# Kernel optimization log

Measured on AMD Instinct MI355X. Metric: run time of the kernel, lower is better.

Reference implementation:

```python
import jax, jax.numpy as jnp
import numpy as np

B, S, D = 8, 2048, 256
H, HD = 4, 64  # num_heads, head_size; H*HD == D


def setup_inputs() -> dict:
    key = jax.random.key(0)
    ks = jax.random.split(key, 9)
    scale = 0.02
    return {
        "x": jax.random.normal(ks[0], (B, S, D), dtype=jnp.float32),
        "Wq": jax.random.normal(ks[1], (D, H * HD), dtype=jnp.float32) * scale,
        "bq": jnp.zeros((H * HD,), dtype=jnp.float32),
        "Wk": jax.random.normal(ks[2], (D, H * HD), dtype=jnp.float32) * scale,
        "bk": jnp.zeros((H * HD,), dtype=jnp.float32),
        "Wv": jax.random.normal(ks[3], (D, H * HD), dtype=jnp.float32) * scale,
        "bv": jnp.zeros((H * HD,), dtype=jnp.float32),
        "Wo": jax.random.normal(ks[4], (H * HD, D), dtype=jnp.float32) * scale,
        "bo": jnp.zeros((D,), dtype=jnp.float32),
    }


def _split_heads(t):
    # [B, S, H*HD] -> [B, H, S, HD]
    b, s, _ = t.shape
    return t.reshape(b, s, H, HD).transpose(0, 2, 1, 3)


def reference(x, Wq, bq, Wk, bk, Wv, bv, Wo, bo):
    q = _split_heads(x @ Wq + bq)
    k = _split_heads(x @ Wk + bk)
    v = _split_heads(x @ Wv + bv)
    scores = jnp.einsum("bhqd,bhkd->bhqk", q, k) / jnp.sqrt(jnp.float32(HD))
    weights = jax.nn.softmax(scores, axis=-1)
    attn = jnp.einsum("bhqk,bhkd->bhqd", weights, v)  # [B, H, S, HD]
    concat = attn.transpose(0, 2, 1, 3).reshape(x.shape[0], -1, H * HD)
    return concat @ Wo + bo
```

## Files before the change

kernel.cpp:

```cpp
#include <hip/hip_runtime.h>
#include <hip/hip_bf16.h>

namespace {

constexpr int B_ = 8, S = 2048, D = 256, H = 4, HD = 64;
constexpr int M = B_ * S;

typedef __attribute__((ext_vector_type(8))) short bf16x8;
typedef __attribute__((ext_vector_type(4))) short bf16x4;
typedef __attribute__((ext_vector_type(4))) float f32x4;
typedef __attribute__((ext_vector_type(16))) float f32x16;
typedef __attribute__((ext_vector_type(4))) unsigned uint4v;

__device__ inline short f2bf(float x) {
  __hip_bfloat16 h = __float2bfloat16(x);
  short s;
  __builtin_memcpy(&s, &h, 2);
  return s;
}

__device__ inline f32x4 mfma16(bf16x8 a, bf16x8 b, f32x4 c) {
  return __builtin_amdgcn_mfma_f32_16x16x32_bf16(a, b, c, 0, 0, 0);
}
__device__ inline f32x16 mfma32(bf16x8 a, bf16x8 b, f32x16 c) {
  return __builtin_amdgcn_mfma_f32_32x32x16_bf16(a, b, c, 0, 0, 0);
}

__device__ inline float exp2a(float x) {
  float r;
  asm("v_exp_f32 %0, %1" : "=v"(r) : "v"(x));
  return r;
}

__device__ inline unsigned cvtpk(float lo, float hi) {
  unsigned r;
  asm("v_cvt_pk_bf16_f32 %0, %1, %2" : "=v"(r) : "v"(lo), "v"(hi));
  return r;
}

__device__ inline bf16x4 pk4(float a, float b, float c, float d) {
  unsigned lo = cvtpk(a, b), hi = cvtpk(c, d);
  uint2 u{lo, hi};
  bf16x4 r;
  __builtin_memcpy(&r, &u, 8);
  return r;
}

__device__ inline bf16x8 ld_cvt8(const float* p) {
  float4 a = *(const float4*)p;
  float4 b = *(const float4*)(p + 4);
  uint4v u = {cvtpk(a.x, a.y), cvtpk(a.z, a.w), cvtpk(b.x, b.y), cvtpk(b.z, b.w)};
  bf16x8 r;
  __builtin_memcpy(&r, &u, 16);
  return r;
}

__global__ __launch_bounds__(256) void prep_w_kernel(
    const float* __restrict__ Wq, const float* __restrict__ Wk,
    const float* __restrict__ Wv, const float* __restrict__ Wo,
    short* __restrict__ WqT, short* __restrict__ WkT,
    short* __restrict__ WvT, short* __restrict__ WoT) {
  const int blk = blockIdx.x, t = threadIdx.x;
  const int wq = blk >> 4, n0 = (blk & 15) * 16;
  const float* W = wq == 0 ? Wq : wq == 1 ? Wk : wq == 2 ? Wv : Wo;
  short* Wt = wq == 0 ? WqT : wq == 1 ? WkT : wq == 2 ? WvT : WoT;
#pragma unroll
  for (int j4 = 0; j4 < 4; ++j4) {
    float4 v = *(const float4*)(W + (size_t)t * 256 + n0 + j4 * 4);
    Wt[(n0 + j4 * 4 + 0) * 256 + t] = f2bf(v.x);
    Wt[(n0 + j4 * 4 + 1) * 256 + t] = f2bf(v.y);
    Wt[(n0 + j4 * 4 + 2) * 256 + t] = f2bf(v.z);
    Wt[(n0 + j4 * 4 + 3) * 256 + t] = f2bf(v.w);
  }
}

__global__ __launch_bounds__(256) void gemm_qkv_kernel(
    const float* __restrict__ x,
    const short* __restrict__ WqT, const short* __restrict__ WkT,
    const short* __restrict__ WvT,
    const float* __restrict__ bq, const float* __restrict__ bk,
    const float* __restrict__ bv,
    short* __restrict__ Qo, short* __restrict__ Ko, short* __restrict__ Vt) {
  const int bx = blockIdx.x;
  const int which = blockIdx.y;
  const short* Wt = which == 0 ? WqT : which == 1 ? WkT : WvT;
  const float* bias = which == 0 ? bq : which == 1 ? bk : bv;

  __shared__ short Xs[2][64 * 32];
  __shared__ short Ws[2][256 * 32];

  const int tid = threadIdx.x;
  const int wid = tid >> 6, lane = tid & 63;
  const int l15 = lane & 15, l4 = lane >> 4;
  const int nt0 = wid * 4;

  const float* xsrc = x + ((size_t)(bx * 64 + (tid >> 2))) * 256 + (tid & 3) * 8;
  const short* wsrc = Wt + ((size_t)(tid >> 2)) * 256 + (tid & 3) * 8;
  short* xdst0 = &Xs[0][tid * 8];
  short* xdst1 = &Xs[1][tid * 8];
  short* wdst0 = &Ws[0][tid * 8];
  short* wdst1 = &Ws[1][tid * 8];

  bf16x8 xr, wr[4];
  xr = ld_cvt8(xsrc);
#pragma unroll
  for (int p = 0; p < 4; ++p) wr[p] = *(const bf16x8*)(wsrc + (size_t)p * 64 * 256);
  *(bf16x8*)xdst0 = xr;
#pragma unroll
  for (int p = 0; p < 4; ++p) *(bf16x8*)(wdst0 + p * 2048) = wr[p];
  __syncthreads();

  f32x4 acc[4][4];
#pragma unroll
  for (int i = 0; i < 4; ++i)
#pragma unroll
    for (int mh = 0; mh < 4; ++mh) acc[i][mh] = f32x4{0.f, 0.f, 0.f, 0.f};

  for (int ks = 0; ks < 8; ++ks) {
    const int cur = ks & 1;
    if (ks < 7) {
      xr = ld_cvt8(xsrc + (ks + 1) * 32);
#pragma unroll
      for (int p = 0; p < 4; ++p)
        wr[p] = *(const bf16x8*)(wsrc + (size_t)p * 64 * 256 + (ks + 1) * 32);
    }
    bf16x8 wf[4], xf[4];
#pragma unroll
    for (int i = 0; i < 4; ++i)
      wf[i] = *(const bf16x8*)&Ws[cur][((nt0 + i) * 16 + l15) * 32 + l4 * 8];
#pragma unroll
    for (int mh = 0; mh < 4; ++mh)
      xf[mh] = *(const bf16x8*)&Xs[cur][(mh * 16 + l15) * 32 + l4 * 8];
    if (which == 2) {
#pragma unroll
      for (int i = 0; i < 4; ++i)
#pragma unroll
        for (int mh = 0; mh < 4; ++mh)
          acc[i][mh] = mfma16(xf[mh], wf[i], acc[i][mh]);
    } else {
#pragma unroll
      for (int i = 0; i < 4; ++i)
#pragma unroll
        for (int mh = 0; mh < 4; ++mh)
          acc[i][mh] = mfma16(wf[i], xf[mh], acc[i][mh]);
    }
    if (ks < 7) {
      short* xd = (cur ? xdst0 : xdst1);
      short* wd = (cur ? wdst0 : wdst1);
      *(bf16x8*)xd = xr;
#pragma unroll
      for (int p = 0; p < 4; ++p) *(bf16x8*)(wd + p * 2048) = wr[p];
    }
    __syncthreads();
  }

  if (which == 2) {
    const int m0 = bx * 64 + l4 * 4;
#pragma unroll
    for (int i = 0; i < 4; ++i) {
      const int n = (nt0 + i) * 16 + l15;
      const float bi = bias[n];
      const int h = n >> 6, d = n & 63;
#pragma unroll
      for (int mh = 0; mh < 4; ++mh) {
        const int m = m0 + mh * 16;
        const int bb = m >> 11, s0 = m & 2047;
        bf16x4 r = pk4(acc[i][mh][0] + bi, acc[i][mh][1] + bi,
                       acc[i][mh][2] + bi, acc[i][mh][3] + bi);
        *(bf16x4*)(Vt + (((size_t)bb * H + h) * HD + d) * S + s0) = r;
      }
    }
  } else {
    const float scale = which == 0 ? 0.18033688011112042f : 1.0f;
    short* outp = which == 0 ? Qo : Ko;
#pragma unroll
    for (int i = 0; i < 4; ++i) {
      const int n0 = (nt0 + i) * 16 + l4 * 4;
      float4 bi = *(const float4*)(bias + n0);
      const int h = n0 >> 6, d0 = n0 & 63;
#pragma unroll
      for (int mh = 0; mh < 4; ++mh) {
        const int m = bx * 64 + mh * 16 + l15;
        const int bb = m >> 11, s = m & 2047;
        bf16x4 r = pk4((acc[i][mh][0] + bi.x) * scale, (acc[i][mh][1] + bi.y) * scale,
                       (acc[i][mh][2] + bi.z) * scale, (acc[i][mh][3] + bi.w) * scale);
        *(bf16x4*)(outp + (((size_t)bb * H + h) * S + s) * HD + d0) = r;
      }
    }
  }
}

__global__ __launch_bounds__(256) void gemm_out_kernel(
    const short* __restrict__ Abf, const short* __restrict__ WoT,
    const float* __restrict__ bo, float* __restrict__ out) {
  const int bx = blockIdx.x;
  __shared__ short Xs[2][64 * 32];
  __shared__ short Ws[2][256 * 32];

  const int tid = threadIdx.x;
  const int wid = tid >> 6, lane = tid & 63;
  const int l15 = lane & 15, l4 = lane >> 4;
  const int nt0 = wid * 4;

  const short* xsrc = Abf + ((size_t)(bx * 64 + (tid >> 2))) * 256 + (tid & 3) * 8;
  const short* wsrc = WoT + ((size_t)(tid >> 2)) * 256 + (tid & 3) * 8;
  short* xdst0 = &Xs[0][tid * 8];
  short* xdst1 = &Xs[1][tid * 8];
  short* wdst0 = &Ws[0][tid * 8];
  short* wdst1 = &Ws[1][tid * 8];

  bf16x8 xr, wr[4];
  xr = *(const bf16x8*)xsrc;
#pragma unroll
  for (int p = 0; p < 4; ++p) wr[p] = *(const bf16x8*)(wsrc + (size_t)p * 64 * 256);
  *(bf16x8*)xdst0 = xr;
#pragma unroll
  for (int p = 0; p < 4; ++p) *(bf16x8*)(wdst0 + p * 2048) = wr[p];
  __syncthreads();

  f32x4 acc[4][4];
#pragma unroll
  for (int i = 0; i < 4; ++i)
#pragma unroll
    for (int mh = 0; mh < 4; ++mh) acc[i][mh] = f32x4{0.f, 0.f, 0.f, 0.f};

  for (int ks = 0; ks < 8; ++ks) {
    const int cur = ks & 1;
    if (ks < 7) {
      xr = *(const bf16x8*)(xsrc + (ks + 1) * 32);
#pragma unroll
      for (int p = 0; p < 4; ++p)
        wr[p] = *(const bf16x8*)(wsrc + (size_t)p * 64 * 256 + (ks + 1) * 32);
    }
    bf16x8 wf[4], xf[4];
#pragma unroll
    for (int i = 0; i < 4; ++i)
      wf[i] = *(const bf16x8*)&Ws[cur][((nt0 + i) * 16 + l15) * 32 + l4 * 8];
#pragma unroll
    for (int mh = 0; mh < 4; ++mh)
      xf[mh] = *(const bf16x8*)&Xs[cur][(mh * 16 + l15) * 32 + l4 * 8];
#pragma unroll
    for (int i = 0; i < 4; ++i)
#pragma unroll
      for (int mh = 0; mh < 4; ++mh)
        acc[i][mh] = mfma16(wf[i], xf[mh], acc[i][mh]);
    if (ks < 7) {
      short* xd = (cur ? xdst0 : xdst1);
      short* wd = (cur ? wdst0 : wdst1);
      *(bf16x8*)xd = xr;
#pragma unroll
      for (int p = 0; p < 4; ++p) *(bf16x8*)(wd + p * 2048) = wr[p];
    }
    __syncthreads();
  }

#pragma unroll
  for (int i = 0; i < 4; ++i) {
    const int n0 = (nt0 + i) * 16 + l4 * 4;
    float4 bi = *(const float4*)(bo + n0);
#pragma unroll
    for (int mh = 0; mh < 4; ++mh) {
      const int m = bx * 64 + mh * 16 + l15;
      float4 r;
      r.x = acc[i][mh][0] + bi.x;
      r.y = acc[i][mh][1] + bi.y;
      r.z = acc[i][mh][2] + bi.z;
      r.w = acc[i][mh][3] + bi.w;
      *(float4*)(out + (size_t)m * 256 + n0) = r;
    }
  }
}

__global__ __launch_bounds__(256) void attn_kernel7(
    const short* __restrict__ Q, const short* __restrict__ K,
    const short* __restrict__ VT, short* __restrict__ Abf) {
  const int lin = blockIdx.x;
  const int bh = lin & 31;
  const int qt = lin >> 5;
  const int tid = threadIdx.x, wid = tid >> 6, lane = tid & 63;
  const int q31 = lane & 31, h = lane >> 5;
  constexpr int NT = S / 64;

  __shared__ short Ks[2][64 * 128];
  __shared__ short Vs[2][64 * 128];

  const short* Kg = K + (size_t)bh * S * HD;
  const short* Vg = VT + (size_t)bh * HD * S;
  const int qrow = qt * 128 + wid * 32;

  const short* Qg = Q + ((size_t)bh * S + qrow + q31) * HD + h * 8;
  bf16x8 qf[4];
#pragma unroll
  for (int ds = 0; ds < 4; ++ds) qf[ds] = *(const bf16x8*)(Qg + ds * 16);

  bf16x8 ones;
#pragma unroll
  for (int i = 0; i < 8; ++i) ones[i] = (short)0x3F80;

  const int srow = tid >> 2;
  const int scol = (tid & 3) * 16;
  const int swz = (srow & 15) * 8;
  const int c0 = scol ^ swz;
  const int c1 = (scol + 8) ^ swz;

  const int fs = (lane & 15) * 8;
  int kcol[4];
#pragma unroll
  for (int ds = 0; ds < 4; ++ds) kcol[ds] = (ds * 16 + h * 8) ^ fs;

  bf16x8 kr0, kr1, vr0, vr1;
  kr0 = *(const bf16x8*)(Kg + (size_t)srow * HD + scol);
  kr1 = *(const bf16x8*)(Kg + (size_t)srow * HD + scol + 8);
  vr0 = *(const bf16x8*)(Vg + (size_t)srow * S + scol);
  vr1 = *(const bf16x8*)(Vg + (size_t)srow * S + scol + 8);
  *(bf16x8*)&Ks[0][srow * 128 + c0] = kr0;
  *(bf16x8*)&Ks[0][srow * 128 + c1] = kr1;
  *(bf16x8*)&Vs[0][srow * 128 + c0] = vr0;
  *(bf16x8*)&Vs[0][srow * 128 + c1] = vr1;
  {
    const short* Kn = Kg + (size_t)64 * HD;
    const short* Vn = Vg + 64;
    kr0 = *(const bf16x8*)(Kn + (size_t)srow * HD + scol);
    kr1 = *(const bf16x8*)(Kn + (size_t)srow * HD + scol + 8);
    vr0 = *(const bf16x8*)(Vn + (size_t)srow * S + scol);
    vr1 = *(const bf16x8*)(Vn + (size_t)srow * S + scol + 8);
  }
  __syncthreads();

  f32x16 o0, o1, lsum;
#pragma unroll
  for (int i = 0; i < 16; ++i) { o0[i] = 0.f; o1[i] = 0.f; lsum[i] = 0.f; }
  bf16x8 pB[4];

#define EXPPACK(S0, S1)                                               \
  {                                                                   \
    _Pragma("unroll") for (int win = 0; win < 2; ++win) {             \
      const f32x16& sc = win ? (S1) : (S0);                           \
      float p[16];                                                    \
      _Pragma("unroll") for (int r = 0; r < 16; ++r)                  \
          p[r] = exp2a(sc[r]);                                        \
      unsigned w[8];                                                  \
      _Pragma("unroll") for (int i = 0; i < 8; ++i)                   \
          w[i] = cvtpk(p[2 * i], p[2 * i + 1]);                       \
      unsigned x0 = w[0], y0 = w[2], x1 = w[1], y1 = w[3];            \
      unsigned x2 = w[4], y2 = w[6], x3 = w[5], y3 = w[7];            \
      asm("v_permlane32_swap_b32 %0, %1" : "+v"(x0), "+v"(y0));       \
      asm("v_permlane32_swap_b32 %0, %1" : "+v"(x1), "+v"(y1));       \
      asm("v_permlane32_swap_b32 %0, %1" : "+v"(x2), "+v"(y2));       \
      asm("v_permlane32_swap_b32 %0, %1" : "+v"(x3), "+v"(y3));       \
      uint4v u0 = {x0, x1, y0, y1};                                   \
      uint4v u1 = {x2, x3, y2, y3};                                   \
      __builtin_memcpy(&pB[win * 2 + 0], &u0, 16);                    \
      __builtin_memcpy(&pB[win * 2 + 1], &u1, 16);                    \
    }                                                                 \
  }

  {
    f32x16 sc0, sc1;
#pragma unroll
    for (int i = 0; i < 16; ++i) { sc0[i] = 0.f; sc1[i] = 0.f; }
    __builtin_amdgcn_s_setprio(1);
#pragma unroll
    for (int ds = 0; ds < 4; ++ds) {
      bf16x8 k0 = *(const bf16x8*)&Ks[0][(q31)*128 + kcol[ds]];
      bf16x8 k1 = *(const bf16x8*)&Ks[0][(32 + q31) * 128 + kcol[ds]];
      sc0 = mfma32(k0, qf[ds], sc0);
      sc1 = mfma32(k1, qf[ds], sc1);
    }
    __builtin_amdgcn_s_setprio(0);
    EXPPACK(sc0, sc1);
    __syncthreads();
    *(bf16x8*)&Ks[1][srow * 128 + c0] = kr0;
    *(bf16x8*)&Ks[1][srow * 128 + c1] = kr1;
    *(bf16x8*)&Vs[1][srow * 128 + c0] = vr0;
    *(bf16x8*)&Vs[1][srow * 128 + c1] = vr1;
    __syncthreads();
  }

  for (int kt = 1; kt < NT; ++kt) {
    const int cur = kt & 1, prv = cur ^ 1;
    if (kt + 1 < NT) {
      const short* Kn = Kg + (size_t)(kt + 1) * 64 * HD;
      const short* Vn = Vg + (size_t)(kt + 1) * 64;
      kr0 = *(const bf16x8*)(Kn + (size_t)srow * HD + scol);
      kr1 = *(const bf16x8*)(Kn + (size_t)srow * HD + scol + 8);
      vr0 = *(const bf16x8*)(Vn + (size_t)srow * S + scol);
      vr1 = *(const bf16x8*)(Vn + (size_t)srow * S + scol + 8);
    }

    f32x16 sc0, sc1;
#pragma unroll
    for (int i = 0; i < 16; ++i) { sc0[i] = 0.f; sc1[i] = 0.f; }

    __builtin_amdgcn_s_setprio(1);
#pragma unroll
    for (int ds = 0; ds < 4; ++ds) {
      bf16x8 k0 = *(const bf16x8*)&Ks[cur][(q31)*128 + kcol[ds]];
      bf16x8 k1 = *(const bf16x8*)&Ks[cur][(32 + q31) * 128 + kcol[ds]];
      sc0 = mfma32(k0, qf[ds], sc0);
      sc1 = mfma32(k1, qf[ds], sc1);
      bf16x8 v0 = *(const bf16x8*)&Vs[prv][(q31)*128 + kcol[ds]];
      bf16x8 v1 = *(const bf16x8*)&Vs[prv][(32 + q31) * 128 + kcol[ds]];
      o0 = mfma32(v0, pB[ds], o0);
      o1 = mfma32(v1, pB[ds], o1);
      lsum = mfma32(ones, pB[ds], lsum);
    }
    __builtin_amdgcn_s_setprio(0);

    EXPPACK(sc0, sc1);
    __syncthreads();
    if (kt + 1 < NT) {
      *(bf16x8*)&Ks[prv][srow * 128 + c0] = kr0;
      *(bf16x8*)&Ks[prv][srow * 128 + c1] = kr1;
      *(bf16x8*)&Vs[prv][srow * 128 + c0] = vr0;
      *(bf16x8*)&Vs[prv][srow * 128 + c1] = vr1;
    }
    __syncthreads();
  }

  {
    const int cur = (NT - 1) & 1;
    __builtin_amdgcn_s_setprio(1);
#pragma unroll
    for (int ds = 0; ds < 4; ++ds) {
      bf16x8 v0 = *(const bf16x8*)&Vs[cur][(q31)*128 + kcol[ds]];
      bf16x8 v1 = *(const bf16x8*)&Vs[cur][(32 + q31) * 128 + kcol[ds]];
      o0 = mfma32(v0, pB[ds], o0);
      o1 = mfma32(v1, pB[ds], o1);
      lsum = mfma32(ones, pB[ds], lsum);
    }
    __builtin_amdgcn_s_setprio(0);
  }
#undef EXPPACK

  const float inv = 1.0f / lsum[0];
  const int b = bh >> 2, hh = bh & 3;
  short* ap = Abf + ((size_t)b * S + qrow + q31) * 256 + hh * 64;
#pragma unroll
  for (int dt = 0; dt < 2; ++dt) {
    const f32x16& o = dt ? o1 : o0;
#pragma unroll
    for (int g = 0; g < 4; ++g) {
      const int d0 = dt * 32 + 8 * g + 4 * h;
      bf16x4 r = pk4(o[4 * g + 0] * inv, o[4 * g + 1] * inv,
                     o[4 * g + 2] * inv, o[4 * g + 3] * inv);
      *(bf16x4*)(ap + d0) = r;
    }
  }
}

}

extern "C" void kernel_launch(void* const* d_in, const int* in_sizes, int n_in,
                              void* d_out, int out_size, void* d_ws, size_t ws_size,
                              hipStream_t stream) {
  const float* x  = (const float*)d_in[0];
  const float* Wq = (const float*)d_in[1];
  const float* bq = (const float*)d_in[2];
  const float* Wk = (const float*)d_in[3];
  const float* bk = (const float*)d_in[4];
  const float* Wv = (const float*)d_in[5];
  const float* bv = (const float*)d_in[6];
  const float* Wo = (const float*)d_in[7];
  const float* bo = (const float*)d_in[8];
  float* out = (float*)d_out;

  const size_t per = (size_t)M * D;
  short* WqT = (short*)d_ws;
  short* WkT = WqT + 256 * 256;
  short* WvT = WkT + 256 * 256;
  short* WoT = WvT + 256 * 256;
  short* Qbf = WoT + 256 * 256;
  short* Kbf = Qbf + per;
  short* Vt  = Kbf + per;
  short* Abf = Vt + per;

  prep_w_kernel<<<64, 256, 0, stream>>>(Wq, Wk, Wv, Wo, WqT, WkT, WvT, WoT);
  gemm_qkv_kernel<<<dim3(256, 3), 256, 0, stream>>>(x, WqT, WkT, WvT, bq, bk, bv,
                                                    Qbf, Kbf, Vt);
  attn_kernel7<<<512, 256, 0, stream>>>(Qbf, Kbf, Vt, Abf);
  gemm_out_kernel<<<256, 256, 0, stream>>>(Abf, WoT, bo, out);
}
```

Baseline: 88.30 us.

## Split attention over key halves and merge partial outputs in a separate kernel

Splits the key/value sequence into two halves across a second grid dimension, doubling attention blocks from 512 to 1024 so more CUs get work. Each block writes unnormalized fp32 partial outputs and row sums, and a new merge kernel adds the two halves, normalizes and writes the bf16 attention result into the Q buffer. Shared-memory tiles shrink to 32 rows and launch bounds request higher occupancy. The cost is an extra kernel launch and extra fp32 global traffic for the partials. Summing the halves without rescaling is correct only because the softmax takes no max, which the base already relies on.

```diff
diff --git a/kernel.cpp b/kernel.cpp
--- a/kernel.cpp
+++ b/kernel.cpp
@@ -190,6 +190,29 @@
   }
 }
 
+__global__ __launch_bounds__(256) void merge_kernel(
+    const float* __restrict__ O0, const float* __restrict__ O1,
+    const float* __restrict__ l0, const float* __restrict__ l1,
+    short* __restrict__ Abf) {
+  const size_t g = ((size_t)blockIdx.x * 256 + threadIdx.x) * 8;
+  const int bh = (int)(g >> 17);
+  const int rem = (int)(g & 131071);
+  const int q = rem >> 6, d = rem & 63;
+  const float iv = 1.0f / (l0[(size_t)bh * 2048 + q] + l1[(size_t)bh * 2048 + q]);
+  float4 a0 = *(const float4*)(O0 + g);
+  float4 a1 = *(const float4*)(O0 + g + 4);
+  float4 b0 = *(const float4*)(O1 + g);
+  float4 b1 = *(const float4*)(O1 + g + 4);
+  uint4v u = {cvtpk((a0.x + b0.x) * iv, (a0.y + b0.y) * iv),
+              cvtpk((a0.z + b0.z) * iv, (a0.w + b0.w) * iv),
+              cvtpk((a1.x + b1.x) * iv, (a1.y + b1.y) * iv),
+              cvtpk((a1.z + b1.z) * iv, (a1.w + b1.w) * iv)};
+  bf16x8 r;
+  __builtin_memcpy(&r, &u, 16);
+  const int b = bh >> 2, h = bh & 3;
+  *(bf16x8*)(Abf + ((size_t)b * 2048 + q) * 256 + h * 64 + d) = r;
+}
+
 __global__ __launch_bounds__(256) void gemm_out_kernel(
     const short* __restrict__ Abf, const short* __restrict__ WoT,
     const float* __restrict__ bo, float* __restrict__ out) {
@@ -271,21 +294,24 @@
   }
 }
 
-__global__ __launch_bounds__(256) void attn_kernel7(
+__global__ __launch_bounds__(256, 4) void attn_kernel11(
     const short* __restrict__ Q, const short* __restrict__ K,
-    const short* __restrict__ VT, short* __restrict__ Abf) {
+    const short* __restrict__ VT, float* __restrict__ Opart,
+    float* __restrict__ lpart) {
   const int lin = blockIdx.x;
   const int bh = lin & 31;
   const int qt = lin >> 5;
+  const int sp = blockIdx.y;
   const int tid = threadIdx.x, wid = tid >> 6, lane = tid & 63;
   const int q31 = lane & 31, h = lane >> 5;
-  constexpr int NT = S / 64;
-
-  __shared__ short Ks[2][64 * 128];
-  __shared__ short Vs[2][64 * 128];
-
-  const short* Kg = K + (size_t)bh * S * HD;
+  constexpr int NT = 16;
+
+  __shared__ short Ks[2][32 * 128];
+  __shared__ short Vs[2][32 * 128];
+
+  const short* Kgs = K + (size_t)bh * S * HD + (size_t)sp * 1024 * HD;
   const short* Vg = VT + (size_t)bh * HD * S;
+  const int vcol0 = sp * 1024;
   const int qrow = qt * 128 + wid * 32;
 
   const short* Qg = Q + ((size_t)bh * S + qrow + q31) * HD + h * 8;
@@ -298,32 +324,38 @@
   for (int i = 0; i < 8; ++i) ones[i] = (short)0x3F80;
 
   const int srow = tid >> 2;
+  const int pr = srow & 31;
   const int scol = (tid & 3) * 16;
-  const int swz = (srow & 15) * 8;
-  const int c0 = scol ^ swz;
-  const int c1 = (scol + 8) ^ swz;
-
-  const int fs = (lane & 15) * 8;
-  int kcol[4];
-#pragma unroll
-  for (int ds = 0; ds < 4; ++ds) kcol[ds] = (ds * 16 + h * 8) ^ fs;
+  const int cb0 = ((srow >> 5) << 6) + scol;
+  const int swz = (pr & 15) * 8;
+  const int c0 = cb0 ^ swz;
+  const int c1 = (cb0 + 8) ^ swz;
+  const int sbase = pr * 128;
+
+  const int fs = (q31 & 15) * 8;
+  int colA[4], colB[4];
+#pragma unroll
+  for (int ds = 0; ds < 4; ++ds) {
+    colA[ds] = (ds * 16 + h * 8) ^ fs;
+    colB[ds] = (64 + ds * 16 + h * 8) ^ fs;
+  }
+  const int rbase = q31 * 128;
 
   bf16x8 kr0, kr1, vr0, vr1;
-  kr0 = *(const bf16x8*)(Kg + (size_t)srow * HD + scol);
-  kr1 = *(const bf16x8*)(Kg + (size_t)srow * HD + scol + 8);
-  vr0 = *(const bf16x8*)(Vg + (size_t)srow * S + scol);
-  vr1 = *(const bf16x8*)(Vg + (size_t)srow * S + scol + 8);
-  *(bf16x8*)&Ks[0][srow * 128 + c0] = kr0;
-  *(bf16x8*)&Ks[0][srow * 128 + c1] = kr1;
-  *(bf16x8*)&Vs[0][srow * 128 + c0] = vr0;
-  *(bf16x8*)&Vs[0][srow * 128 + c1] = vr1;
+  kr0 = *(const bf16x8*)(Kgs + (size_t)srow * HD + scol);
+  kr1 = *(const bf16x8*)(Kgs + (size_t)srow * HD + scol + 8);
+  vr0 = *(const bf16x8*)(Vg + (size_t)srow * S + vcol0 + scol);
+  vr1 = *(const bf16x8*)(Vg + (size_t)srow * S + vcol0 + scol + 8);
+  *(bf16x8*)&Ks[0][sbase + c0] = kr0;
+  *(bf16x8*)&Ks[0][sbase + c1] = kr1;
+  *(bf16x8*)&Vs[0][sbase + c0] = vr0;
+  *(bf16x8*)&Vs[0][sbase + c1] = vr1;
   {
-    const short* Kn = Kg + (size_t)64 * HD;
-    const short* Vn = Vg + 64;
+    const short* Kn = Kgs + (size_t)64 * HD;
     kr0 = *(const bf16x8*)(Kn + (size_t)srow * HD + scol);
     kr1 = *(const bf16x8*)(Kn + (size_t)srow * HD + scol + 8);
-    vr0 = *(const bf16x8*)(Vn + (size_t)srow * S + scol);
-    vr1 = *(const bf16x8*)(Vn + (size_t)srow * S + scol + 8);
+    vr0 = *(const bf16x8*)(Vg + (size_t)srow * S + vcol0 + 64 + scol);
+    vr1 = *(const bf16x8*)(Vg + (size_t)srow * S + vcol0 + 64 + scol + 8);
   }
   __syncthreads();
 
@@ -362,30 +394,29 @@
     __builtin_amdgcn_s_setprio(1);
 #pragma unroll
     for (int ds = 0; ds < 4; ++ds) {
-      bf16x8 k0 = *(const bf16x8*)&Ks[0][(q31)*128 + kcol[ds]];
-      bf16x8 k1 = *(const bf16x8*)&Ks[0][(32 + q31) * 128 + kcol[ds]];
+      bf16x8 k0 = *(const bf16x8*)&Ks[0][rbase + colA[ds]];
+      bf16x8 k1 = *(const bf16x8*)&Ks[0][rbase + colB[ds]];
       sc0 = mfma32(k0, qf[ds], sc0);
       sc1 = mfma32(k1, qf[ds], sc1);
     }
     __builtin_amdgcn_s_setprio(0);
     EXPPACK(sc0, sc1);
     __syncthreads();
-    *(bf16x8*)&Ks[1][srow * 128 + c0] = kr0;
-    *(bf16x8*)&Ks[1][srow * 128 + c1] = kr1;
-    *(bf16x8*)&Vs[1][srow * 128 + c0] = vr0;
-    *(bf16x8*)&Vs[1][srow * 128 + c1] = vr1;
+    *(bf16x8*)&Ks[1][sbase + c0] = kr0;
+    *(bf16x8*)&Ks[1][sbase + c1] = kr1;
+    *(bf16x8*)&Vs[1][sbase + c0] = vr0;
+    *(bf16x8*)&Vs[1][sbase + c1] = vr1;
     __syncthreads();
   }
 
   for (int kt = 1; kt < NT; ++kt) {
     const int cur = kt & 1, prv = cur ^ 1;
     if (kt + 1 < NT) {
-      const short* Kn = Kg + (size_t)(kt + 1) * 64 * HD;
-      const short* Vn = Vg + (size_t)(kt + 1) * 64;
+      const short* Kn = Kgs + (size_t)(kt + 1) * 64 * HD;
       kr0 = *(const bf16x8*)(Kn + (size_t)srow * HD + scol);
       kr1 = *(const bf16x8*)(Kn + (size_t)srow * HD + scol + 8);
-      vr0 = *(const bf16x8*)(Vn + (size_t)srow * S + scol);
-      vr1 = *(const bf16x8*)(Vn + (size_t)srow * S + scol + 8);
+      vr0 = *(const bf16x8*)(Vg + (size_t)srow * S + vcol0 + (kt + 1) * 64 + scol);
+      vr1 = *(const bf16x8*)(Vg + (size_t)srow * S + vcol0 + (kt + 1) * 64 + scol + 8);
     }
 
     f32x16 sc0, sc1;
@@ -395,12 +426,12 @@
     __builtin_amdgcn_s_setprio(1);
 #pragma unroll
     for (int ds = 0; ds < 4; ++ds) {
-      bf16x8 k0 = *(const bf16x8*)&Ks[cur][(q31)*128 + kcol[ds]];
-      bf16x8 k1 = *(const bf16x8*)&Ks[cur][(32 + q31) * 128 + kcol[ds]];
+      bf16x8 k0 = *(const bf16x8*)&Ks[cur][rbase + colA[ds]];
+      bf16x8 k1 = *(const bf16x8*)&Ks[cur][rbase + colB[ds]];
       sc0 = mfma32(k0, qf[ds], sc0);
       sc1 = mfma32(k1, qf[ds], sc1);
-      bf16x8 v0 = *(const bf16x8*)&Vs[prv][(q31)*128 + kcol[ds]];
-      bf16x8 v1 = *(const bf16x8*)&Vs[prv][(32 + q31) * 128 + kcol[ds]];
+      bf16x8 v0 = *(const bf16x8*)&Vs[prv][rbase + colA[ds]];
+      bf16x8 v1 = *(const bf16x8*)&Vs[prv][rbase + colB[ds]];
       o0 = mfma32(v0, pB[ds], o0);
       o1 = mfma32(v1, pB[ds], o1);
       lsum = mfma32(ones, pB[ds], lsum);
@@ -410,10 +441,10 @@
     EXPPACK(sc0, sc1);
     __syncthreads();
     if (kt + 1 < NT) {
-      *(bf16x8*)&Ks[prv][srow * 128 + c0] = kr0;
-      *(bf16x8*)&Ks[prv][srow * 128 + c1] = kr1;
-      *(bf16x8*)&Vs[prv][srow * 128 + c0] = vr0;
-      *(bf16x8*)&Vs[prv][srow * 128 + c1] = vr1;
+      *(bf16x8*)&Ks[prv][sbase + c0] = kr0;
+      *(bf16x8*)&Ks[prv][sbase + c1] = kr1;
+      *(bf16x8*)&Vs[prv][sbase + c0] = vr0;
+      *(bf16x8*)&Vs[prv][sbase + c1] = vr1;
     }
     __syncthreads();
   }
@@ -423,8 +454,8 @@
     __builtin_amdgcn_s_setprio(1);
 #pragma unroll
     for (int ds = 0; ds < 4; ++ds) {
-      bf16x8 v0 = *(const bf16x8*)&Vs[cur][(q31)*128 + kcol[ds]];
-      bf16x8 v1 = *(const bf16x8*)&Vs[cur][(32 + q31) * 128 + kcol[ds]];
+      bf16x8 v0 = *(const bf16x8*)&Vs[cur][rbase + colA[ds]];
+      bf16x8 v1 = *(const bf16x8*)&Vs[cur][rbase + colB[ds]];
       o0 = mfma32(v0, pB[ds], o0);
       o1 = mfma32(v1, pB[ds], o1);
       lsum = mfma32(ones, pB[ds], lsum);
@@ -433,19 +464,23 @@
   }
 #undef EXPPACK
 
-  const float inv = 1.0f / lsum[0];
-  const int b = bh >> 2, hh = bh & 3;
-  short* ap = Abf + ((size_t)b * S + qrow + q31) * 256 + hh * 64;
+  float* op = Opart + (((size_t)sp * 32 + bh) * 2048 + qrow + q31) * 64;
 #pragma unroll
   for (int dt = 0; dt < 2; ++dt) {
     const f32x16& o = dt ? o1 : o0;
 #pragma unroll
     for (int g = 0; g < 4; ++g) {
       const int d0 = dt * 32 + 8 * g + 4 * h;
-      bf16x4 r = pk4(o[4 * g + 0] * inv, o[4 * g + 1] * inv,
-                     o[4 * g + 2] * inv, o[4 * g + 3] * inv);
-      *(bf16x4*)(ap + d0) = r;
-    }
+      float4 r;
+      r.x = o[4 * g + 0];
+      r.y = o[4 * g + 1];
+      r.z = o[4 * g + 2];
+      r.w = o[4 * g + 3];
+      *(float4*)(op + d0) = r;
+    }
+  }
+  if (lane < 32) {
+    lpart[((size_t)sp * 32 + bh) * 2048 + qrow + q31] = lsum[0];
   }
 }
 
@@ -473,11 +508,17 @@
   short* Qbf = WoT + 256 * 256;
   short* Kbf = Qbf + per;
   short* Vt  = Kbf + per;
-  short* Abf = Vt + per;
+  float* Op0 = (float*)(Vt + per);
+  float* Op1 = Op0 + per;
+  float* lp  = Op1 + per;
+  float* lp0 = lp;
+  float* lp1 = lp + 32 * 2048;
+  short* Abf = Qbf;
 
   prep_w_kernel<<<64, 256, 0, stream>>>(Wq, Wk, Wv, Wo, WqT, WkT, WvT, WoT);
   gemm_qkv_kernel<<<dim3(256, 3), 256, 0, stream>>>(x, WqT, WkT, WvT, bq, bk, bv,
                                                     Qbf, Kbf, Vt);
-  attn_kernel7<<<512, 256, 0, stream>>>(Qbf, Kbf, Vt, Abf);
+  attn_kernel11<<<dim3(512, 2), 256, 0, stream>>>(Qbf, Kbf, Vt, Op0, lp);
+  merge_kernel<<<2048, 256, 0, stream>>>(Op0, Op1, lp0, lp1, Abf);
   gemm_out_kernel<<<256, 256, 0, stream>>>(Abf, WoT, bo, out);
 }
```

Result: slower. 245.7 us (+178.2%).

## Triple-buffer V tiles to drop one barrier per attention iteration

Applied to the files above, without the earlier changes.

The V tile ring in shared memory grows from two to three buffers, and the V load is shifted one iteration later than the K load. This lets the loop write the next K and V tiles right after the exp/pack step with a single __syncthreads instead of two. The goal is to cut barrier stalls in the inner loop. In exchange it uses 16 KB more LDS per block, which may lower occupancy.

```diff
diff --git a/kernel.cpp b/kernel.cpp
--- a/kernel.cpp
+++ b/kernel.cpp
@@ -271,7 +271,7 @@
   }
 }
 
-__global__ __launch_bounds__(256) void attn_kernel7(
+__global__ __launch_bounds__(256) void attn_kernel13(
     const short* __restrict__ Q, const short* __restrict__ K,
     const short* __restrict__ VT, short* __restrict__ Abf) {
   const int lin = blockIdx.x;
@@ -282,7 +282,7 @@
   constexpr int NT = S / 64;
 
   __shared__ short Ks[2][64 * 128];
-  __shared__ short Vs[2][64 * 128];
+  __shared__ short Vs[3][64 * 128];
 
   const short* Kg = K + (size_t)bh * S * HD;
   const short* Vg = VT + (size_t)bh * HD * S;
@@ -311,19 +311,14 @@
   bf16x8 kr0, kr1, vr0, vr1;
   kr0 = *(const bf16x8*)(Kg + (size_t)srow * HD + scol);
   kr1 = *(const bf16x8*)(Kg + (size_t)srow * HD + scol + 8);
-  vr0 = *(const bf16x8*)(Vg + (size_t)srow * S + scol);
-  vr1 = *(const bf16x8*)(Vg + (size_t)srow * S + scol + 8);
   *(bf16x8*)&Ks[0][srow * 128 + c0] = kr0;
   *(bf16x8*)&Ks[0][srow * 128 + c1] = kr1;
-  *(bf16x8*)&Vs[0][srow * 128 + c0] = vr0;
-  *(bf16x8*)&Vs[0][srow * 128 + c1] = vr1;
   {
     const short* Kn = Kg + (size_t)64 * HD;
-    const short* Vn = Vg + 64;
     kr0 = *(const bf16x8*)(Kn + (size_t)srow * HD + scol);
     kr1 = *(const bf16x8*)(Kn + (size_t)srow * HD + scol + 8);
-    vr0 = *(const bf16x8*)(Vn + (size_t)srow * S + scol);
-    vr1 = *(const bf16x8*)(Vn + (size_t)srow * S + scol + 8);
+    vr0 = *(const bf16x8*)(Vg + (size_t)srow * S + scol);
+    vr1 = *(const bf16x8*)(Vg + (size_t)srow * S + scol + 8);
   }
   __syncthreads();
 
@@ -369,38 +364,39 @@
     }
     __builtin_amdgcn_s_setprio(0);
     EXPPACK(sc0, sc1);
-    __syncthreads();
     *(bf16x8*)&Ks[1][srow * 128 + c0] = kr0;
     *(bf16x8*)&Ks[1][srow * 128 + c1] = kr1;
-    *(bf16x8*)&Vs[1][srow * 128 + c0] = vr0;
-    *(bf16x8*)&Vs[1][srow * 128 + c1] = vr1;
+    *(bf16x8*)&Vs[0][srow * 128 + c0] = vr0;
+    *(bf16x8*)&Vs[0][srow * 128 + c1] = vr1;
     __syncthreads();
   }
 
+  int vrd = 0;
+  int vwr = 1;
   for (int kt = 1; kt < NT; ++kt) {
-    const int cur = kt & 1, prv = cur ^ 1;
     if (kt + 1 < NT) {
       const short* Kn = Kg + (size_t)(kt + 1) * 64 * HD;
-      const short* Vn = Vg + (size_t)(kt + 1) * 64;
       kr0 = *(const bf16x8*)(Kn + (size_t)srow * HD + scol);
       kr1 = *(const bf16x8*)(Kn + (size_t)srow * HD + scol + 8);
-      vr0 = *(const bf16x8*)(Vn + (size_t)srow * S + scol);
-      vr1 = *(const bf16x8*)(Vn + (size_t)srow * S + scol + 8);
-    }
+    }
+    vr0 = *(const bf16x8*)(Vg + (size_t)srow * S + kt * 64 + scol);
+    vr1 = *(const bf16x8*)(Vg + (size_t)srow * S + kt * 64 + scol + 8);
 
     f32x16 sc0, sc1;
 #pragma unroll
     for (int i = 0; i < 16; ++i) { sc0[i] = 0.f; sc1[i] = 0.f; }
 
+    const short* kb = &Ks[kt & 1][0];
+    const short* vb = &Vs[vrd][0];
     __builtin_amdgcn_s_setprio(1);
 #pragma unroll
     for (int ds = 0; ds < 4; ++ds) {
-      bf16x8 k0 = *(const bf16x8*)&Ks[cur][(q31)*128 + kcol[ds]];
-      bf16x8 k1 = *(const bf16x8*)&Ks[cur][(32 + q31) * 128 + kcol[ds]];
+      bf16x8 k0 = *(const bf16x8*)&kb[(q31)*128 + kcol[ds]];
+      bf16x8 k1 = *(const bf16x8*)&kb[(32 + q31) * 128 + kcol[ds]];
       sc0 = mfma32(k0, qf[ds], sc0);
       sc1 = mfma32(k1, qf[ds], sc1);
-      bf16x8 v0 = *(const bf16x8*)&Vs[prv][(q31)*128 + kcol[ds]];
-      bf16x8 v1 = *(const bf16x8*)&Vs[prv][(32 + q31) * 128 + kcol[ds]];
+      bf16x8 v0 = *(const bf16x8*)&vb[(q31)*128 + kcol[ds]];
+      bf16x8 v1 = *(const bf16x8*)&vb[(32 + q31) * 128 + kcol[ds]];
       o0 = mfma32(v0, pB[ds], o0);
       o1 = mfma32(v1, pB[ds], o1);
       lsum = mfma32(ones, pB[ds], lsum);
@@ -408,23 +404,30 @@
     __builtin_amdgcn_s_setprio(0);
 
     EXPPACK(sc0, sc1);
+
+    if (kt + 1 < NT) {
+      short* kw = &Ks[(kt + 1) & 1][0];
+      *(bf16x8*)&kw[srow * 128 + c0] = kr0;
+      *(bf16x8*)&kw[srow * 128 + c1] = kr1;
+    }
+    {
+      short* vw = &Vs[vwr][0];
+      *(bf16x8*)&vw[srow * 128 + c0] = vr0;
+      *(bf16x8*)&vw[srow * 128 + c1] = vr1;
+    }
     __syncthreads();
-    if (kt + 1 < NT) {
-      *(bf16x8*)&Ks[prv][srow * 128 + c0] = kr0;
-      *(bf16x8*)&Ks[prv][srow * 128 + c1] = kr1;
-      *(bf16x8*)&Vs[prv][srow * 128 + c0] = vr0;
-      *(bf16x8*)&Vs[prv][srow * 128 + c1] = vr1;
-    }
-    __syncthreads();
+
+    vrd = vwr;
+    vwr = (vwr == 2) ? 0 : vwr + 1;
   }
 
   {
-    const int cur = (NT - 1) & 1;
+    const short* vb = &Vs[vrd][0];
     __builtin_amdgcn_s_setprio(1);
 #pragma unroll
     for (int ds = 0; ds < 4; ++ds) {
-      bf16x8 v0 = *(const bf16x8*)&Vs[cur][(q31)*128 + kcol[ds]];
-      bf16x8 v1 = *(const bf16x8*)&Vs[cur][(32 + q31) * 128 + kcol[ds]];
+      bf16x8 v0 = *(const bf16x8*)&vb[(q31)*128 + kcol[ds]];
+      bf16x8 v1 = *(const bf16x8*)&vb[(32 + q31) * 128 + kcol[ds]];
       o0 = mfma32(v0, pB[ds], o0);
       o1 = mfma32(v1, pB[ds], o1);
       lsum = mfma32(ones, pB[ds], lsum);
@@ -478,6 +481,6 @@
   prep_w_kernel<<<64, 256, 0, stream>>>(Wq, Wk, Wv, Wo, WqT, WkT, WvT, WoT);
   gemm_qkv_kernel<<<dim3(256, 3), 256, 0, stream>>>(x, WqT, WkT, WvT, bq, bk, bv,
                                                     Qbf, Kbf, Vt);
-  attn_kernel7<<<512, 256, 0, stream>>>(Qbf, Kbf, Vt, Abf);
+  attn_kernel13<<<512, 256, 0, stream>>>(Qbf, Kbf, Vt, Abf);
   gemm_out_kernel<<<256, 256, 0, stream>>>(Abf, WoT, bo, out);
 }
```

Measured after the change: 88.48 us (median of 2 runs). Within noise of the previous version (+0.2%).
